# Kernel optimization log

Measured on AMD Instinct MI355X. Metric: run time of the kernel, lower is better.

## Reference

```python
import jax, jax.numpy as jnp
import numpy as np

B, S, D_MODEL, H = 4, 2048, 1024, 16
DEPTH = D_MODEL // H          # 64
HD = DEPTH // 2               # 32, per-head projection dim
SCALE = float(np.sqrt(DEPTH))  # note: sqrt(full depth), as in the torch code
NEG = -1e10


def setup_inputs() -> dict:
    key = jax.random.key(0)
    kq, kk, kv, km, kwq, kwk, kwv, kwo = jax.random.split(key, 8)
    q = jax.random.normal(kq, (B, S, D_MODEL), dtype=jnp.float32)
    k = jax.random.normal(kk, (B, S, D_MODEL), dtype=jnp.float32)
    v = jax.random.normal(kv, (B, S, D_MODEL), dtype=jnp.float32)
    attention_mask = jax.random.uniform(km, (B, S, S)) < 0.1
    # xavier-uniform-ish init; stacked per-head weights [H, d_model, hd]
    lim_qkv = float(np.sqrt(6.0 / (D_MODEL + HD)))
    Wq = jax.random.uniform(kwq, (H, D_MODEL, HD), minval=-lim_qkv, maxval=lim_qkv)
    Wk = jax.random.uniform(kwk, (H, D_MODEL, HD), minval=-lim_qkv, maxval=lim_qkv)
    Wv = jax.random.uniform(kwv, (H, D_MODEL, HD), minval=-lim_qkv, maxval=lim_qkv)
    lim_o = float(np.sqrt(6.0 / (H * HD + D_MODEL)))
    Wo = jax.random.uniform(kwo, (H * HD, D_MODEL), minval=-lim_o, maxval=lim_o)
    return {"q": q, "k": k, "v": v, "attention_mask": attention_mask,
            "Wq": Wq, "Wk": Wk, "Wv": Wv, "Wo": Wo}


def reference(q, k, v, attention_mask, Wq, Wk, Wv, Wo):
    # batched per-head projections (equivalent to the per-head Linear loop)
    Q = jnp.einsum('bsd,hde->bhse', q, Wq)   # [B,H,S,hd]
    K = jnp.einsum('bsd,hde->bhse', k, Wk)
    V = jnp.einsum('bsd,hde->bhse', v, Wv)
    scores = jnp.einsum('bhqe,bhke->bhqk', Q, K) / SCALE  # [B,H,S,S]
    scores = jnp.where(attention_mask[:, None, :, :], NEG, scores)
    attn = jax.nn.softmax(scores, axis=-1)
    z = jnp.einsum('bhqk,bhke->bhqe', attn, V)            # [B,H,S,hd]
    # concat heads along last dim (head order matches torch cat)
    multi = z.transpose(0, 2, 1, 3).reshape(q.shape[0], q.shape[1], H * HD)
    out = multi @ Wo                                       # [B,S,d_model]
    return out  # dropout p=0.0 (eval) is identity
```

## Files before the change

kernel.cpp:

```cpp
#include <hip/hip_runtime.h>
#include <hip/hip_bf16.h>
#include <math.h>

typedef unsigned short u16;
typedef unsigned int u32;
typedef unsigned long long u64;
typedef __attribute__((ext_vector_type(8))) short s16x8;
typedef __attribute__((ext_vector_type(4))) short s16x4;
typedef __attribute__((ext_vector_type(4))) float f32x4;
typedef __attribute__((ext_vector_type(16))) float f32x16;
typedef __attribute__((ext_vector_type(2))) unsigned int u32x2;

#define DEV static __device__ __forceinline__

DEV u16 f2bf(float f){
  __hip_bfloat16 h = __float2bfloat16(f);
  return *reinterpret_cast<u16*>(&h);
}

DEV u32 cvt_pk_bf16(float lo, float hi_){
  u32 r;
  asm("v_cvt_pk_bf16_f32 %0, %1, %2" : "=v"(r) : "v"(lo), "v"(hi_));
  return r;
}

DEV u32x2 pl32swap(u32 a, u32 b){
  return __builtin_amdgcn_permlane32_swap(a, b, false, false);
}
DEV float xhalf_sum(float x){
  u32x2 r = pl32swap(__float_as_uint(x), __float_as_uint(x));
  return __uint_as_float(r[0]) + __uint_as_float(r[1]);
}

template<int CPOS> DEV float mzero(float p, u32 msn){
  int ext;
  asm("v_bfe_i32 %0, %1, %2, 1" : "=v"(ext) : "v"(msn), "n"(CPOS));
  return __uint_as_float(__float_as_uint(p) & (u32)ext);
}

__global__ void detect_mask_kernel(const unsigned char* __restrict__ m, int* __restrict__ flag){
  __shared__ int cnt;
  if (threadIdx.x==0) cnt=0;
  __syncthreads();
  int nz=0;
  for (int i=threadIdx.x;i<4096;i+=256) nz += (m[(size_t)i*4+1]!=0)?1:0;
  if (nz) atomicAdd(&cnt, nz);
  __syncthreads();
  if (threadIdx.x==0) *flag = (cnt==0)?4:1;
}

__global__ __launch_bounds__(256) void pack_mask_kernel(const unsigned char* __restrict__ m,
    const int* __restrict__ flag, u16* __restrict__ mb16){
  const int stride = *flag;
  const size_t gid = (size_t)blockIdx.x*256u + threadIdx.x;
  u32 bits = 0;
  if (stride == 1){
    const uint4 v = *(const uint4*)(m + gid*16);
    bits  =  ((v.x & 0x01010101u) * 0x01020408u) >> 24;
    bits |= (((v.y & 0x01010101u) * 0x01020408u) >> 24) << 4;
    bits |= (((v.z & 0x01010101u) * 0x01020408u) >> 24) << 8;
    bits |= (((v.w & 0x01010101u) * 0x01020408u) >> 24) << 12;
  } else {
    const unsigned char* mm = m + gid*64;
    const uint4 a = *(const uint4*)(mm);
    const uint4 b = *(const uint4*)(mm+16);
    const uint4 c = *(const uint4*)(mm+32);
    const uint4 d = *(const uint4*)(mm+48);
    bits  = (u32)(a.x!=0) | ((u32)(a.y!=0)<<1) | ((u32)(a.z!=0)<<2) | ((u32)(a.w!=0)<<3)
          | ((u32)(b.x!=0)<<4) | ((u32)(b.y!=0)<<5) | ((u32)(b.z!=0)<<6) | ((u32)(b.w!=0)<<7)
          | ((u32)(c.x!=0)<<8) | ((u32)(c.y!=0)<<9) | ((u32)(c.z!=0)<<10)| ((u32)(c.w!=0)<<11)
          | ((u32)(d.x!=0)<<12)| ((u32)(d.y!=0)<<13)| ((u32)(d.z!=0)<<14)| ((u32)(d.w!=0)<<15);
  }
  mb16[gid] = (u16)bits;
}

__global__ __launch_bounds__(256) void prep_weights_kernel(
    const float* __restrict__ Wq, const float* __restrict__ Wk, const float* __restrict__ Wv,
    const float* __restrict__ Wo, u16* __restrict__ WT, u16* __restrict__ WoT){
  int gid = blockIdx.x*256 + threadIdx.x;
  if (gid < 3*512*1024){
    int z = gid >> 19;
    int r = gid & ((1<<19)-1);
    int n = r >> 10, d = r & 1023;
    const float* W = (z==0)?Wq:((z==1)?Wk:Wv);
    int h = n>>5, e = n&31;
    float wv = W[((size_t)h*1024 + (size_t)d)*32 + e];
    if (z==0) wv *= 0.18033688011112042f;
    WT[gid] = f2bf(wv);
  } else {
    int r = gid - 3*512*1024;
    int n = r >> 9, cc = r & 511;
    WoT[r] = f2bf(Wo[(size_t)cc*1024 + n]);
  }
}

__global__ __launch_bounds__(256) void gemm_proj_kernel(
    const float* __restrict__ Aq, const float* __restrict__ Ak, const float* __restrict__ Av,
    const u16* __restrict__ WT, u16* __restrict__ Qp, u16* __restrict__ Kp, u16* __restrict__ Vt)
{
  __shared__ u16 As[128*64];
  __shared__ u16 Bs[128*64];
  const int z = blockIdx.z;
  const float* __restrict__ A = (z==0)?Aq:((z==1)?Ak:Av);
  const u16* __restrict__ W = WT + (size_t)z*(512*1024);
  const int m0 = blockIdx.x*128, n0 = blockIdx.y*128;
  const int t = threadIdx.x, lane = t&63, wv = t>>6;
  const int wr = wv>>1, wc = wv&1;
  const int c = lane&15, g = lane>>4;
  f32x4 acc[4][4] = {};
  for (int kk=0; kk<1024; kk+=64){
    #pragma unroll
    for (int j=0;j<8;j++){
      int idx = t + j*256;
      int row = idx>>4, kq=(idx&15)<<2;
      f32x4 a4 = *(const f32x4*)(A + (size_t)(m0+row)*1024 + kk + kq);
      s16x4 b4;
      b4[0]=(short)f2bf(a4[0]); b4[1]=(short)f2bf(a4[1]);
      b4[2]=(short)f2bf(a4[2]); b4[3]=(short)f2bf(a4[3]);
      int co = (kq<<1) ^ ((row&7)<<4);
      *(s16x4*)((char*)As + row*128 + co) = b4;
    }
    #pragma unroll
    for (int j=0;j<4;j++){
      int idx = t + j*256;
      int n = idx>>3, k8=(idx&7)<<3;
      s16x8 bv = *(const s16x8*)(W + (size_t)(n0+n)*1024 + kk + k8);
      int co = (k8<<1) ^ ((n&7)<<4);
      *(s16x8*)((char*)Bs + n*128 + co) = bv;
    }
    __syncthreads();
    #pragma unroll
    for (int ks=0;ks<2;ks++){
      s16x8 af[4], bf[4];
      #pragma unroll
      for (int i=0;i<4;i++){
        int ra = wr*64 + i*16 + c;
        af[i] = *(const s16x8*)((const char*)As + ra*128 + ((ks*64 + g*16) ^ ((ra&7)<<4)));
        int rb = wc*64 + i*16 + c;
        bf[i] = *(const s16x8*)((const char*)Bs + rb*128 + ((ks*64 + g*16) ^ ((rb&7)<<4)));
      }
      #pragma unroll
      for (int mi=0;mi<4;mi++)
        #pragma unroll
        for (int nj=0;nj<4;nj++)
          acc[mi][nj] = __builtin_amdgcn_mfma_f32_16x16x32_bf16(af[mi], bf[nj], acc[mi][nj], 0, 0, 0);
    }
    __syncthreads();
  }
  #pragma unroll
  for (int mi=0;mi<4;mi++){
    #pragma unroll
    for (int nj=0;nj<4;nj++){
      #pragma unroll
      for (int r=0;r<4;r++){
        int gm = m0 + wr*64 + mi*16 + g*4 + r;
        int gn = n0 + wc*64 + nj*16 + c;
        u16 val = f2bf(acc[mi][nj][r]);
        int b = gm>>11, s = gm&2047, hh = gn>>5, e = gn&31;
        if (z==0)      Qp[((size_t)(b*16+hh)*2048 + s)*32 + e] = val;
        else if (z==1) Kp[((size_t)(b*16+hh)*2048 + s)*32 + e] = val;
        else           Vt[((size_t)(b*16+hh)*32 + e)*2048 + s] = val;
      }
    }
  }
}

__global__ __launch_bounds__(256, 4) void attn_kernel(
    const u16* __restrict__ Qp, const u16* __restrict__ Kp, const u16* __restrict__ Vt,
    const u32* __restrict__ mb32, u16* __restrict__ Z)
{
  __shared__ float Osh[4][32][36];
  const int t = threadIdx.x, lane = t&63, wid = t>>6;
  const int c = lane&31, hi = lane>>5;
  const int hi8 = hi*8;
  const int wg = blockIdx.x;
  const int xcd = wg & 7, loc = wg >> 3;
  const int bh = xcd*8 + (loc>>4);
  const int qb = loc & 15;
  const int b = bh>>4, h = bh&15;
  const int q0 = qb*128 + wid*32;
  const u16* Qh = Qp + (size_t)bh*2048*32;
  const u16* Kh = Kp + (size_t)bh*2048*32;
  const u16* Vh = Vt + (size_t)bh*32*2048;

  const s16x8 qf0 = *(const s16x8*)(Qh + (size_t)(q0 + c)*32 + hi8);
  const s16x8 qf1 = *(const s16x8*)(Qh + (size_t)(q0 + c)*32 + 16 + hi8);

  const f32x16 z16 = {0,0,0,0,0,0,0,0,0,0,0,0,0,0,0,0};
  f32x16 OA = z16, OB = z16;
  f32x4 LA = {0,0,0,0}, LB = {0,0,0,0};
  const u32* mrowp = mb32 + ((size_t)b*2048 + (size_t)(q0 + c))*64;

  for (int kt = 0; kt < 64; kt += 2){
    const int kbA = kt*32, kbB = kbA + 32;
    const u16* kbaseA = Kh + (size_t)(kbA + c)*32 + hi8;
    const s16x8 kfA0 = *(const s16x8*)(kbaseA);
    const s16x8 kfA1 = *(const s16x8*)(kbaseA + 16);
    const u16* kbaseB = Kh + (size_t)(kbB + c)*32 + hi8;
    const s16x8 kfB0 = *(const s16x8*)(kbaseB);
    const s16x8 kfB1 = *(const s16x8*)(kbaseB + 16);
    const u16* vbase = Vh + (size_t)c*2048 + kbA + hi8;
    const s16x8 vfA0 = *(const s16x8*)(vbase);
    const s16x8 vfA1 = *(const s16x8*)(vbase + 16);
    const s16x8 vfB0 = *(const s16x8*)(vbase + 32);
    const s16x8 vfB1 = *(const s16x8*)(vbase + 48);
    const u64 mw = *(const u64*)(mrowp + kt);
    const u32 msnA = ~(((u32)mw) >> (4*hi));
    const u32 msnB = ~(((u32)(mw >> 32)) >> (4*hi));

    f32x16 pA = __builtin_amdgcn_mfma_f32_32x32x16_bf16(kfA0, qf0, z16, 0, 0, 0);
    pA = __builtin_amdgcn_mfma_f32_32x32x16_bf16(kfA1, qf1, pA, 0, 0, 0);
    f32x16 pB = __builtin_amdgcn_mfma_f32_32x32x16_bf16(kfB0, qf0, z16, 0, 0, 0);
    pB = __builtin_amdgcn_mfma_f32_32x32x16_bf16(kfB1, qf1, pB, 0, 0, 0);

    #define MZE(P,R,MS) P[R] = mzero<(((R)&3)+8*((R)>>2))>(__builtin_amdgcn_exp2f(P[R]), MS)
    MZE(pA,0,msnA);  MZE(pA,1,msnA);  MZE(pA,2,msnA);  MZE(pA,3,msnA);
    MZE(pA,4,msnA);  MZE(pA,5,msnA);  MZE(pA,6,msnA);  MZE(pA,7,msnA);
    MZE(pA,8,msnA);  MZE(pA,9,msnA);  MZE(pA,10,msnA); MZE(pA,11,msnA);
    MZE(pA,12,msnA); MZE(pA,13,msnA); MZE(pA,14,msnA); MZE(pA,15,msnA);
    MZE(pB,0,msnB);  MZE(pB,1,msnB);  MZE(pB,2,msnB);  MZE(pB,3,msnB);
    MZE(pB,4,msnB);  MZE(pB,5,msnB);  MZE(pB,6,msnB);  MZE(pB,7,msnB);
    MZE(pB,8,msnB);  MZE(pB,9,msnB);  MZE(pB,10,msnB); MZE(pB,11,msnB);
    MZE(pB,12,msnB); MZE(pB,13,msnB); MZE(pB,14,msnB); MZE(pB,15,msnB);
    #undef MZE

    #pragma unroll
    for (int i=0;i<4;i++){
      LA[i] += (pA[i] + pA[i+4]) + (pA[i+8] + pA[i+12]);
      LB[i] += (pB[i] + pB[i+4]) + (pB[i+8] + pB[i+12]);
    }

    u32 pwA0 = cvt_pk_bf16(pA[0],  pA[1]);
    u32 pwA1 = cvt_pk_bf16(pA[2],  pA[3]);
    u32 pwA2 = cvt_pk_bf16(pA[4],  pA[5]);
    u32 pwA3 = cvt_pk_bf16(pA[6],  pA[7]);
    u32 pwA4 = cvt_pk_bf16(pA[8],  pA[9]);
    u32 pwA5 = cvt_pk_bf16(pA[10], pA[11]);
    u32 pwA6 = cvt_pk_bf16(pA[12], pA[13]);
    u32 pwA7 = cvt_pk_bf16(pA[14], pA[15]);
    u32x2 a02 = pl32swap(pwA0, pwA2);
    u32x2 a13 = pl32swap(pwA1, pwA3);
    u32x2 a46 = pl32swap(pwA4, pwA6);
    u32x2 a57 = pl32swap(pwA5, pwA7);
    union { u32 u[4]; s16x8 v; } fA0 = {{a02[0], a13[0], a02[1], a13[1]}};
    union { u32 u[4]; s16x8 v; } fA1 = {{a46[0], a57[0], a46[1], a57[1]}};
    u32 pwB0 = cvt_pk_bf16(pB[0],  pB[1]);
    u32 pwB1 = cvt_pk_bf16(pB[2],  pB[3]);
    u32 pwB2 = cvt_pk_bf16(pB[4],  pB[5]);
    u32 pwB3 = cvt_pk_bf16(pB[6],  pB[7]);
    u32 pwB4 = cvt_pk_bf16(pB[8],  pB[9]);
    u32 pwB5 = cvt_pk_bf16(pB[10], pB[11]);
    u32 pwB6 = cvt_pk_bf16(pB[12], pB[13]);
    u32 pwB7 = cvt_pk_bf16(pB[14], pB[15]);
    u32x2 b02 = pl32swap(pwB0, pwB2);
    u32x2 b13 = pl32swap(pwB1, pwB3);
    u32x2 b46 = pl32swap(pwB4, pwB6);
    u32x2 b57 = pl32swap(pwB5, pwB7);
    union { u32 u[4]; s16x8 v; } fB0 = {{b02[0], b13[0], b02[1], b13[1]}};
    union { u32 u[4]; s16x8 v; } fB1 = {{b46[0], b57[0], b46[1], b57[1]}};

    OA = __builtin_amdgcn_mfma_f32_32x32x16_bf16(vfA0, fA0.v, OA, 0, 0, 0);
    OA = __builtin_amdgcn_mfma_f32_32x32x16_bf16(vfA1, fA1.v, OA, 0, 0, 0);
    OB = __builtin_amdgcn_mfma_f32_32x32x16_bf16(vfB0, fB0.v, OB, 0, 0, 0);
    OB = __builtin_amdgcn_mfma_f32_32x32x16_bf16(vfB1, fB1.v, OB, 0, 0, 0);
  }

  const float lown = ((LA[0]+LB[0]) + (LA[1]+LB[1])) + ((LA[2]+LB[2]) + (LA[3]+LB[3]));
  const float linv = 1.0f / xhalf_sum(lown);
  #pragma unroll
  for (int r=0;r<16;r++){
    const int hd = (r&3) + 8*(r>>2) + 4*hi;
    Osh[wid][c][hd] = (OA[r] + OB[r]) * linv;
  }
  __syncthreads();
  const int rq = lane >> 1, rc0 = (lane & 1)*16;
  const float* orow = &Osh[wid][rq][0];
  union { u16 q[8]; s16x8 v; } o0, o1;
  #pragma unroll
  for (int j=0;j<8;j++){ o0.q[j] = f2bf(orow[rc0+j]); o1.q[j] = f2bf(orow[rc0+8+j]); }
  u16* zp = Z + ((size_t)b*2048 + (size_t)(q0 + rq))*512 + h*32 + rc0;
  *(s16x8*)(zp)   = o0.v;
  *(s16x8*)(zp+8) = o1.v;
}

__global__ __launch_bounds__(256) void gemm_out_kernel(
    const u16* __restrict__ Zb, const u16* __restrict__ WoT, float* __restrict__ out)
{
  __shared__ u16 As[128*64];
  __shared__ u16 Bs[128*64];
  const int m0 = blockIdx.x*128, n0 = blockIdx.y*128;
  const int t = threadIdx.x, lane=t&63, wv=t>>6;
  const int wr=wv>>1, wc=wv&1, c=lane&15, g=lane>>4;
  f32x4 acc[4][4] = {};
  for (int kk=0; kk<512; kk+=64){
    #pragma unroll
    for (int j=0;j<4;j++){
      int idx = t + j*256;
      int row = idx>>3, k8=(idx&7)<<3;
      int co = (k8<<1) ^ ((row&7)<<4);
      s16x8 av = *(const s16x8*)(Zb + (size_t)(m0+row)*512 + kk + k8);
      *(s16x8*)((char*)As + row*128 + co) = av;
      s16x8 bv = *(const s16x8*)(WoT + (size_t)(n0+row)*512 + kk + k8);
      *(s16x8*)((char*)Bs + row*128 + co) = bv;
    }
    __syncthreads();
    #pragma unroll
    for (int ks=0;ks<2;ks++){
      s16x8 af[4], bf[4];
      #pragma unroll
      for (int i=0;i<4;i++){
        int ra = wr*64 + i*16 + c;
        af[i] = *(const s16x8*)((const char*)As + ra*128 + ((ks*64 + g*16) ^ ((ra&7)<<4)));
        int rb = wc*64 + i*16 + c;
        bf[i] = *(const s16x8*)((const char*)Bs + rb*128 + ((ks*64 + g*16) ^ ((rb&7)<<4)));
      }
      #pragma unroll
      for (int mi=0;mi<4;mi++)
        #pragma unroll
        for (int nj=0;nj<4;nj++)
          acc[mi][nj] = __builtin_amdgcn_mfma_f32_16x16x32_bf16(af[mi], bf[nj], acc[mi][nj], 0, 0, 0);
    }
    __syncthreads();
  }
  #pragma unroll
  for (int mi=0;mi<4;mi++)
    #pragma unroll
    for (int nj=0;nj<4;nj++)
      #pragma unroll
      for (int r=0;r<4;r++){
        int gm = m0 + wr*64 + mi*16 + g*4 + r;
        int gn = n0 + wc*64 + nj*16 + c;
        out[(size_t)gm*1024 + gn] = acc[mi][nj][r];
      }
}

extern "C" void kernel_launch(void* const* d_in, const int* in_sizes, int n_in,
                              void* d_out, int out_size, void* d_ws, size_t ws_size,
                              hipStream_t stream)
{
  const float* q  = (const float*)d_in[0];
  const float* k  = (const float*)d_in[1];
  const float* v  = (const float*)d_in[2];
  const unsigned char* mask = (const unsigned char*)d_in[3];
  const float* Wq = (const float*)d_in[4];
  const float* Wk = (const float*)d_in[5];
  const float* Wv = (const float*)d_in[6];
  const float* Wo = (const float*)d_in[7];
  float* out = (float*)d_out;

  char* ws = (char*)d_ws;
  u16* Qp  = (u16*)(ws);
  u16* Kp  = (u16*)(ws + 8388608);
  u16* Vt  = (u16*)(ws + 16777216);
  u16* Z   = (u16*)(ws + 25165824);
  u16* WT  = (u16*)(ws + 33554432);
  u16* WoT = (u16*)(ws + 36700160);
  u16* mb16 = (u16*)(ws + 37748736);
  int* flag = (int*)(ws + 39845888);

  detect_mask_kernel<<<1, 256, 0, stream>>>(mask, flag);
  pack_mask_kernel<<<4096, 256, 0, stream>>>(mask, flag, mb16);
  prep_weights_kernel<<<8192, 256, 0, stream>>>(Wq, Wk, Wv, Wo, WT, WoT);
  gemm_proj_kernel<<<dim3(64,4,3), 256, 0, stream>>>(q, k, v, WT, Qp, Kp, Vt);
  attn_kernel<<<1024, 256, 0, stream>>>(Qp, Kp, Vt, (const u32*)mb16, Z);
  gemm_out_kernel<<<dim3(64,8), 256, 0, stream>>>(Z, WoT, out);
  (void)in_sizes; (void)n_in; (void)out_size; (void)ws_size;
}
```

Baseline: 207.3 us.

## Split attention key range across wave pairs and combine partial sums in LDS

Each attention block now handles 64 queries with two waves per 32-query tile, each wave processing half the key range. Partial outputs and normalizer sums from the second wave are passed through shared memory and merged by the first before normalization and store. The grid doubles to 2048 blocks to expose more parallelism and shorten each wave's serial loop, at the cost of an extra barrier, LDS traffic, and half the waves idling in the epilogue.

```diff
diff --git a/kernel.cpp b/kernel.cpp
--- a/kernel.cpp
+++ b/kernel.cpp
@@ -169,16 +169,19 @@
     const u16* __restrict__ Qp, const u16* __restrict__ Kp, const u16* __restrict__ Vt,
     const u32* __restrict__ mb32, u16* __restrict__ Z)
 {
-  __shared__ float Osh[4][32][36];
+  __shared__ float Psh[2][32][33];
+  __shared__ float Tsh[2][32][33];
+  __shared__ float Lsh[2][32];
   const int t = threadIdx.x, lane = t&63, wid = t>>6;
   const int c = lane&31, hi = lane>>5;
   const int hi8 = hi*8;
+  const int qt = wid>>1, kh = wid&1;
   const int wg = blockIdx.x;
   const int xcd = wg & 7, loc = wg >> 3;
-  const int bh = xcd*8 + (loc>>4);
-  const int qb = loc & 15;
+  const int bh = xcd*8 + (loc>>5);
+  const int qg = loc & 31;
   const int b = bh>>4, h = bh&15;
-  const int q0 = qb*128 + wid*32;
+  const int q0 = qg*64 + qt*32;
   const u16* Qh = Qp + (size_t)bh*2048*32;
   const u16* Kh = Kp + (size_t)bh*2048*32;
   const u16* Vh = Vt + (size_t)bh*32*2048;
@@ -190,8 +193,9 @@
   f32x16 OA = z16, OB = z16;
   f32x4 LA = {0,0,0,0}, LB = {0,0,0,0};
   const u32* mrowp = mb32 + ((size_t)b*2048 + (size_t)(q0 + c))*64;
-
-  for (int kt = 0; kt < 64; kt += 2){
+  const int kt0 = kh*32;
+
+  for (int kt = kt0; kt < kt0 + 32; kt += 2){
     const int kbA = kt*32, kbB = kbA + 32;
     const u16* kbaseA = Kh + (size_t)(kbA + c)*32 + hi8;
     const s16x8 kfA0 = *(const s16x8*)(kbaseA);
@@ -266,21 +270,35 @@
   }
 
   const float lown = ((LA[0]+LB[0]) + (LA[1]+LB[1])) + ((LA[2]+LB[2]) + (LA[3]+LB[3]));
-  const float linv = 1.0f / xhalf_sum(lown);
-  #pragma unroll
-  for (int r=0;r<16;r++){
-    const int hd = (r&3) + 8*(r>>2) + 4*hi;
-    Osh[wid][c][hd] = (OA[r] + OB[r]) * linv;
+  if (kh == 1){
+    #pragma unroll
+    for (int r=0;r<16;r++){
+      const int hd = (r&3) + 8*(r>>2) + 4*hi;
+      Psh[qt][c][hd] = OA[r] + OB[r];
+    }
+    const float s1 = xhalf_sum(lown);
+    if (hi == 0) Lsh[qt][c] = s1;
   }
   __syncthreads();
-  const int rq = lane >> 1, rc0 = (lane & 1)*16;
-  const float* orow = &Osh[wid][rq][0];
-  union { u16 q[8]; s16x8 v; } o0, o1;
-  #pragma unroll
-  for (int j=0;j<8;j++){ o0.q[j] = f2bf(orow[rc0+j]); o1.q[j] = f2bf(orow[rc0+8+j]); }
-  u16* zp = Z + ((size_t)b*2048 + (size_t)(q0 + rq))*512 + h*32 + rc0;
-  *(s16x8*)(zp)   = o0.v;
-  *(s16x8*)(zp+8) = o1.v;
+  if (kh == 0){
+    const float linv = 1.0f / (xhalf_sum(lown) + Lsh[qt][c]);
+    #pragma unroll
+    for (int r=0;r<16;r++){
+      const int hd = (r&3) + 8*(r>>2) + 4*hi;
+      Tsh[qt][c][hd] = ((OA[r] + OB[r]) + Psh[qt][c][hd]) * linv;
+    }
+  }
+  __syncthreads();
+  if (kh == 0){
+    const int rq = lane >> 1, rc0 = (lane & 1)*16;
+    const float* orow = &Tsh[qt][rq][0];
+    union { u16 q[8]; s16x8 v; } o0, o1;
+    #pragma unroll
+    for (int j=0;j<8;j++){ o0.q[j] = f2bf(orow[rc0+j]); o1.q[j] = f2bf(orow[rc0+8+j]); }
+    u16* zp = Z + ((size_t)b*2048 + (size_t)(q0 + rq))*512 + h*32 + rc0;
+    *(s16x8*)(zp)   = o0.v;
+    *(s16x8*)(zp+8) = o1.v;
+  }
 }
 
 __global__ __launch_bounds__(256) void gemm_out_kernel(
@@ -362,7 +380,7 @@
   pack_mask_kernel<<<4096, 256, 0, stream>>>(mask, flag, mb16);
   prep_weights_kernel<<<8192, 256, 0, stream>>>(Wq, Wk, Wv, Wo, WT, WoT);
   gemm_proj_kernel<<<dim3(64,4,3), 256, 0, stream>>>(q, k, v, WT, Qp, Kp, Vt);
-  attn_kernel<<<1024, 256, 0, stream>>>(Qp, Kp, Vt, (const u32*)mb16, Z);
+  attn_kernel<<<2048, 256, 0, stream>>>(Qp, Kp, Vt, (const u32*)mb16, Z);
   gemm_out_kernel<<<dim3(64,8), 256, 0, stream>>>(Z, WoT, out);
   (void)in_sizes; (void)n_in; (void)out_size; (void)ws_size;
 }
```

Measured after the change: 214.4 us. 3.4% more time.
